# Kernel optimization log

Hardware: AMD Instinct MI355X
Metric: run time of the kernel (lower is better)

## Reference

```python
import jax, jax.numpy as jnp
import numpy as np

F_BINS, T_STEPS, N_ACTIONS = 257, 65536, 256  # STFT bins, frames, codebook size


def setup_inputs() -> dict:
    key = jax.random.key(0)
    k1, k2, k3, k4 = jax.random.split(key, 4)
    x_out = jax.random.normal(k1, (F_BINS, T_STEPS), dtype=jnp.float32)
    x_source = jax.random.normal(k2, (F_BINS, T_STEPS), dtype=jnp.float32)
    x_clean = jax.random.normal(k3, (F_BINS, T_STEPS), dtype=jnp.float32)
    # G is self.G_mat = G_mat.T, i.e. [freq, action]; gains in [0,1)
    G = jax.random.uniform(k4, (F_BINS, N_ACTIONS), dtype=jnp.float32)
    return {"x_out": x_out, "x_source": x_source, "x_clean": x_clean, "G": G}


def reference(x_out, x_source, x_clean, G):
    # sums[t, a] = sum_f (x_clean[f, t] - G[f, a] * x_source[f, t])
    #            = sum_f x_clean[:, t]  -  (x_source^T @ G)[t, a]
    clean_sum = jnp.sum(x_clean, axis=0)                 # [T]
    proj = jnp.einsum('ft,fa->ta', x_source, G)          # [T, A]
    sums = clean_sum[:, None] - proj                     # [T, A]
    A_t = jnp.argmin(sums, axis=1)                       # [T], values in [0, A)
    F, T = x_source.shape
    # Faithful to the original loop: wiener_true[:, a] = G[:, a] for each
    # SELECTED ACTION a (column indexed by action id, not timestep).
    # Duplicate indices write identical values, so scatter-set is well-defined.
    wiener_true = jnp.zeros((F, T), dtype=x_source.dtype).at[:, A_t].set(G[:, A_t])
    true_out = (wiener_true * x_source).T                # [T, F]
    loss = jnp.mean((true_out - x_out.T) ** 2)
    return loss
```

## Files before the change

kernel.cpp:

```cpp
#include <hip/hip_runtime.h>

#define F_BINS  257
#define T_STEPS 65536
#define N_ACT   256
#define TM      128
#define NBLK_G  512
#define NTHR    256
#define XO_PB   8224

typedef float f32x4 __attribute__((ext_vector_type(4)));
typedef short s16x8 __attribute__((ext_vector_type(8)));
typedef unsigned u32x4 __attribute__((ext_vector_type(4)));

#define WS_PART  1024
#define WS_CORR  20480
#define WS_MASK  24576
#define WS_GFRAG 65536

__device__ __forceinline__ unsigned short f2bf_rne(float x) {
  unsigned u = __builtin_bit_cast(unsigned, x);
  return (unsigned short)((u + 0x7FFFu + ((u >> 16) & 1u)) >> 16);
}
__device__ __forceinline__ unsigned pack_bf(float hi, float lo) {
  return __builtin_amdgcn_perm(__builtin_bit_cast(unsigned, hi),
                               __builtin_bit_cast(unsigned, lo), 0x07060302u);
}

__global__ __launch_bounds__(256) void k_prep(const float* __restrict__ G,
                                              unsigned char* __restrict__ gfrag) {
  const int u = blockIdx.x * 256 + threadIdx.x;
  const int lane = u & 63, ng = (u >> 6) & 15, kk = u >> 10;
  const int r16 = lane & 15, g = lane >> 4;
  const int a = ng * 16 + r16;
  unsigned short h[8];
#pragma unroll
  for (int j = 0; j < 8; ++j) {
    const int f = kk * 32 + 8 * g + j;
    h[j] = (f < F_BINS) ? f2bf_rne(G[f * N_ACT + a]) : (unsigned short)0;
  }
  u32x4 w;
#pragma unroll
  for (int i = 0; i < 4; ++i)
    w[i] = (unsigned)h[2 * i] | ((unsigned)h[2 * i + 1] << 16);
  *(u32x4*)(gfrag + (size_t)u * 16) = w;
}

__global__ __launch_bounds__(NTHR, 2) void k_gemm(
    const float* __restrict__ xs, const float4* __restrict__ xo4,
    const unsigned char* __restrict__ gfrag,
    unsigned* __restrict__ maskp, double* __restrict__ partial) {
  const int tid = threadIdx.x, lane = tid & 63, wv = tid >> 6;
  const int g = lane >> 4, r16 = lane & 15;
  const int t0 = blockIdx.x * TM;
  const int tcol = t0 + 32 * wv + 2 * r16;

  __shared__ __align__(16) unsigned char Bh[73728];
  __shared__ unsigned lmask[8];
  __shared__ double sdw[4];
  if (tid < 8) lmask[tid] = 0u;

#define STAGE_BH(hv)                                                          \
  {                                                                           \
    _Pragma("unroll") for (int idx = 0; idx < 18; ++idx) {                    \
      const int j = 18 * wv + idx;                      \
      const int kkc = j >> 3, ic = j & 7;                                     \
      const unsigned char* src = gfrag +                                      \
          (size_t)(kkc * 16 + 8 * (hv) + ic) * 1024 + (size_t)lane * 16;      \
      unsigned char* dst = &Bh[j * 1024];                                     \
      __builtin_amdgcn_global_load_lds(                                       \
          (const __attribute__((address_space(1))) unsigned*)src,             \
          (__attribute__((address_space(3))) unsigned*)dst, 16, 0, 0);        \
    }                                                                         \
  }
#define LOADB(slot, kkv)                                                      \
  {                                                                           \
    _Pragma("unroll") for (int j = 0; j < 8; ++j) {                           \
      int f = 32 * (kkv) + 8 * g + j;                                         \
      if ((kkv) == 8) f = f > 256 ? 256 : f;   \
      va[slot][j] = *(const float2*)(xs + (size_t)f * T_STEPS + tcol);        \
    }                                                                         \
  }

  float2 va[4][8];
  LOADB(0, 0) LOADB(1, 1) LOADB(2, 2) LOADB(3, 3)
  __builtin_amdgcn_sched_barrier(0);
  STAGE_BH(0)
  __builtin_amdgcn_sched_barrier(0);

  s16x8 af[9][2];
#pragma unroll
  for (int kk = 0; kk < 9; ++kk) {
    const int b = kk & 3;
    af[kk][0] = __builtin_bit_cast(s16x8, (u32x4){
        pack_bf(va[b][1].x, va[b][0].x), pack_bf(va[b][3].x, va[b][2].x),
        pack_bf(va[b][5].x, va[b][4].x), pack_bf(va[b][7].x, va[b][6].x)});
    af[kk][1] = __builtin_bit_cast(s16x8, (u32x4){
        pack_bf(va[b][1].y, va[b][0].y), pack_bf(va[b][3].y, va[b][2].y),
        pack_bf(va[b][5].y, va[b][4].y), pack_bf(va[b][7].y, va[b][6].y)});
    if (kk + 4 <= 8) LOADB(b, kk + 4)
  }
#undef LOADB

  __syncthreads();

  float bv[2][4]; int bc[2][4];
#pragma unroll
  for (int h = 0; h < 2; ++h) {
    if (h == 1) {
      __syncthreads();
      STAGE_BH(1)
      __syncthreads();
    }
    f32x4 acc[2][8];
#pragma unroll
    for (int tau = 0; tau < 2; ++tau)
#pragma unroll
      for (int n = 0; n < 8; ++n) acc[tau][n] = (f32x4){0.f, 0.f, 0.f, 0.f};
#pragma unroll
    for (int kk = 0; kk < 9; ++kk) {
      const unsigned char* bp = &Bh[(kk * 8 * 64 + lane) * 16];
#pragma unroll
      for (int n = 0; n < 8; ++n) {
        const s16x8 bfr = *(const s16x8*)(bp + n * 1024);
        acc[0][n] = __builtin_amdgcn_mfma_f32_16x16x32_bf16(
            af[kk][0], bfr, acc[0][n], 0, 0, 0);
        acc[1][n] = __builtin_amdgcn_mfma_f32_16x16x32_bf16(
            af[kk][1], bfr, acc[1][n], 0, 0, 0);
      }
    }
#pragma unroll
    for (int n = 0; n < 8; ++n) {
      const int c = 128 * h + 16 * n + r16;
#pragma unroll
      for (int tau = 0; tau < 2; ++tau)
#pragma unroll
        for (int q = 0; q < 4; ++q) {
          const float v = acc[tau][n][q];
          if (h == 0 && n == 0) { bv[tau][q] = v; bc[tau][q] = c; }
          else if (v > bv[tau][q]) { bv[tau][q] = v; bc[tau][q] = c; }
        }
    }
  }
#undef STAGE_BH

  const float4* xop = xo4 + (size_t)blockIdx.x * XO_PB + tid;
  float4 xv[2][8];
#pragma unroll
  for (int j = 0; j < 8; ++j) xv[0][j] = xop[j * 256];
#pragma unroll
  for (int j = 0; j < 8; ++j) xv[1][j] = xop[2048 + j * 256];
  float4 wrem = (float4){0.f, 0.f, 0.f, 0.f};
  if (tid < 32) wrem = xo4[(size_t)blockIdx.x * XO_PB + 8192 + tid];

#pragma unroll
  for (int m = 1; m <= 8; m <<= 1) {
#pragma unroll
    for (int tau = 0; tau < 2; ++tau)
#pragma unroll
      for (int q = 0; q < 4; ++q) {
        const float ov = __shfl_xor(bv[tau][q], m);
        const int   oc = __shfl_xor(bc[tau][q], m);
        if (ov > bv[tau][q] || (ov == bv[tau][q] && oc < bc[tau][q])) {
          bv[tau][q] = ov; bc[tau][q] = oc;
        }
      }
  }
  if (r16 == 0) {
#pragma unroll
    for (int tau = 0; tau < 2; ++tau)
#pragma unroll
      for (int q = 0; q < 4; ++q)
        atomicOr(&lmask[bc[tau][q] >> 5], 1u << (bc[tau][q] & 31));
  }
  __syncthreads();
  if (tid < 8) maskp[blockIdx.x * 8 + tid] = lmask[tid];

  double ds = 0.0;
#pragma unroll
  for (int r = 0; r < 4; ++r) {
    float fs = 0.f;
#pragma unroll
    for (int j = 0; j < 8; ++j) {
      const float4 v = xv[r & 1][j];
      fs = fmaf(v.x, v.x, fs); fs = fmaf(v.y, v.y, fs);
      fs = fmaf(v.z, v.z, fs); fs = fmaf(v.w, v.w, fs);
    }
    ds += (double)fs;
    if (r + 2 < 4) {
#pragma unroll
      for (int j = 0; j < 8; ++j)
        xv[r & 1][j] = xop[(size_t)(r + 2) * 2048 + j * 256];
    }
  }
  {
    float fs = 0.f;
    fs = fmaf(wrem.x, wrem.x, fs); fs = fmaf(wrem.y, wrem.y, fs);
    fs = fmaf(wrem.z, wrem.z, fs); fs = fmaf(wrem.w, wrem.w, fs);
    ds += (double)fs;
  }
#pragma unroll
  for (int off = 32; off; off >>= 1) ds += __shfl_down(ds, off);
  if (lane == 0) sdw[wv] = ds;
  __syncthreads();
  if (tid == 0) partial[blockIdx.x] = sdw[0] + sdw[1] + sdw[2] + sdw[3];
}

__global__ __launch_bounds__(256) void k_corr(
    const float* __restrict__ xs, const float* __restrict__ xo,
    const float* __restrict__ G, const unsigned* __restrict__ maskp,
    double* __restrict__ corrp) {
  __shared__ unsigned m8[8];
  const int tid = threadIdx.x;
  if (tid < 8) m8[tid] = 0u;
  __syncthreads();
  unsigned m = 0;
  for (int b = tid >> 3; b < NBLK_G; b += 32) m |= maskp[b * 8 + (tid & 7)];
  atomicOr(&m8[tid & 7], m);
  __syncthreads();
  const int f = blockIdx.x, a = tid;
  const bool sel = (m8[a >> 5] >> (a & 31)) & 1u;
  const float gv  = G[f * N_ACT + a];
  const float xsv = xs[(size_t)f * T_STEPS + a];
  const float xov = xo[(size_t)f * T_STEPS + a];
  const float gx  = gv * xsv;
  double acc = sel ? (double)(gx * (gx - 2.f * xov)) : 0.0;
#pragma unroll
  for (int off = 32; off; off >>= 1) acc += __shfl_down(acc, off);
  __shared__ double sdc[4];
  if ((tid & 63) == 0) sdc[tid >> 6] = acc;
  __syncthreads();
  if (tid == 0) corrp[f] = sdc[0] + sdc[1] + sdc[2] + sdc[3];
}

__global__ __launch_bounds__(256) void k_final(const double* __restrict__ partial,
                                               const double* __restrict__ corrp,
                                               float* __restrict__ out) {
  const int tid = threadIdx.x;
  double s = partial[tid] + partial[tid + 256] + corrp[tid];
  if (tid == 0) s += corrp[256];
#pragma unroll
  for (int off = 32; off; off >>= 1) s += __shfl_down(s, off);
  __shared__ double sd[4];
  if ((tid & 63) == 0) sd[tid >> 6] = s;
  __syncthreads();
  if (tid == 0)
    out[0] = (float)((sd[0] + sd[1] + sd[2] + sd[3]) /
                     ((double)F_BINS * (double)T_STEPS));
}

extern "C" void kernel_launch(void* const* d_in, const int* in_sizes, int n_in,
                              void* d_out, int out_size, void* d_ws, size_t ws_size,
                              hipStream_t stream) {
  const float* x_out    = (const float*)d_in[0];
  const float* x_source = (const float*)d_in[1];
  const float* G        = (const float*)d_in[3];

  char* ws = (char*)d_ws;
  double*        partial = (double*)(ws + WS_PART);
  double*        corrp   = (double*)(ws + WS_CORR);
  unsigned*      maskp   = (unsigned*)(ws + WS_MASK);
  unsigned char* gfrag   = (unsigned char*)(ws + WS_GFRAG);

  k_prep <<<36, 256, 0, stream>>>(G, gfrag);
  k_gemm <<<NBLK_G, NTHR, 0, stream>>>(x_source, (const float4*)x_out,
                                       gfrag, maskp, partial);
  k_corr <<<F_BINS, 256, 0, stream>>>(x_source, x_out, G, maskp, corrp);
  k_final<<<1, 256, 0, stream>>>(partial, corrp, (float*)d_out);
}
```

Before: 40.63 us.

## Precompute per-action correction terms in prep kernel and drop separate corr kernel

The per-action correction term no longer depends on the selection mask, so it is now computed ahead of the GEMM in extra blocks of the prep kernel, as partial sums over groups of 17 frequency bins. The mask is applied only in the final single-block reduction, which sums the 16 partial rows per action. This removes one kernel launch (the 257-block corr kernel) and its serial dependency after the GEMM. In exchange the final kernel does a bit more work and the prep kernel reads more data.

```diff
diff --git a/kernel.cpp b/kernel.cpp
--- a/kernel.cpp
+++ b/kernel.cpp
@@ -7,14 +7,16 @@
 #define NBLK_G  512
 #define NTHR    256
 #define XO_PB   8224
+#define PREP_BLKS 36
+#define CORR_BLKS 16
 
 typedef float f32x4 __attribute__((ext_vector_type(4)));
 typedef short s16x8 __attribute__((ext_vector_type(8)));
 typedef unsigned u32x4 __attribute__((ext_vector_type(4)));
 
 #define WS_PART  1024
-#define WS_CORR  20480
-#define WS_MASK  24576
+#define WS_CPART 8192
+#define WS_MASK  40960
 #define WS_GFRAG 65536
 
 __device__ __forceinline__ unsigned short f2bf_rne(float x) {
@@ -26,23 +28,42 @@
                                __builtin_bit_cast(unsigned, lo), 0x07060302u);
 }
 
-__global__ __launch_bounds__(256) void k_prep(const float* __restrict__ G,
-                                              unsigned char* __restrict__ gfrag) {
-  const int u = blockIdx.x * 256 + threadIdx.x;
-  const int lane = u & 63, ng = (u >> 6) & 15, kk = u >> 10;
-  const int r16 = lane & 15, g = lane >> 4;
-  const int a = ng * 16 + r16;
-  unsigned short h[8];
-#pragma unroll
-  for (int j = 0; j < 8; ++j) {
-    const int f = kk * 32 + 8 * g + j;
-    h[j] = (f < F_BINS) ? f2bf_rne(G[f * N_ACT + a]) : (unsigned short)0;
-  }
-  u32x4 w;
-#pragma unroll
-  for (int i = 0; i < 4; ++i)
-    w[i] = (unsigned)h[2 * i] | ((unsigned)h[2 * i + 1] << 16);
-  *(u32x4*)(gfrag + (size_t)u * 16) = w;
+__global__ __launch_bounds__(256) void k_pre(
+    const float* __restrict__ G, const float* __restrict__ xs,
+    const float* __restrict__ xo, unsigned char* __restrict__ gfrag,
+    double* __restrict__ cpart) {
+  const int tid = threadIdx.x;
+  if (blockIdx.x < PREP_BLKS) {
+    const int u = blockIdx.x * 256 + tid;
+    const int lane = u & 63, ng = (u >> 6) & 15, kk = u >> 10;
+    const int r16 = lane & 15, g = lane >> 4;
+    const int a = ng * 16 + r16;
+    unsigned short h[8];
+#pragma unroll
+    for (int j = 0; j < 8; ++j) {
+      const int f = kk * 32 + 8 * g + j;
+      h[j] = (f < F_BINS) ? f2bf_rne(G[f * N_ACT + a]) : (unsigned short)0;
+    }
+    u32x4 w;
+#pragma unroll
+    for (int i = 0; i < 4; ++i)
+      w[i] = (unsigned)h[2 * i] | ((unsigned)h[2 * i + 1] << 16);
+    *(u32x4*)(gfrag + (size_t)u * 16) = w;
+    return;
+  }
+  const int b = blockIdx.x - PREP_BLKS;
+  const int a = tid;
+  const int f0 = b * 17;
+  const int f1 = f0 + 17 > F_BINS ? F_BINS : f0 + 17;
+  double ca = 0.0;
+  for (int f = f0; f < f1; ++f) {
+    const float gv  = G[f * N_ACT + a];
+    const float xsv = xs[(size_t)f * T_STEPS + a];
+    const float xov = xo[(size_t)f * T_STEPS + a];
+    const float gx  = gv * xsv;
+    ca += (double)(gx * (gx - 2.f * xov));
+  }
+  cpart[b * 256 + a] = ca;
 }
 
 __global__ __launch_bounds__(NTHR, 2) void k_gemm(
@@ -205,10 +226,9 @@
   if (tid == 0) partial[blockIdx.x] = sdw[0] + sdw[1] + sdw[2] + sdw[3];
 }
 
-__global__ __launch_bounds__(256) void k_corr(
-    const float* __restrict__ xs, const float* __restrict__ xo,
-    const float* __restrict__ G, const unsigned* __restrict__ maskp,
-    double* __restrict__ corrp) {
+__global__ __launch_bounds__(256) void k_final(
+    const double* __restrict__ partial, const double* __restrict__ cpart,
+    const unsigned* __restrict__ maskp, float* __restrict__ out) {
   __shared__ unsigned m8[8];
   const int tid = threadIdx.x;
   if (tid < 8) m8[tid] = 0u;
@@ -217,27 +237,12 @@
   for (int b = tid >> 3; b < NBLK_G; b += 32) m |= maskp[b * 8 + (tid & 7)];
   atomicOr(&m8[tid & 7], m);
   __syncthreads();
-  const int f = blockIdx.x, a = tid;
+  const int a = tid;
   const bool sel = (m8[a >> 5] >> (a & 31)) & 1u;
-  const float gv  = G[f * N_ACT + a];
-  const float xsv = xs[(size_t)f * T_STEPS + a];
-  const float xov = xo[(size_t)f * T_STEPS + a];
-  const float gx  = gv * xsv;
-  double acc = sel ? (double)(gx * (gx - 2.f * xov)) : 0.0;
-#pragma unroll
-  for (int off = 32; off; off >>= 1) acc += __shfl_down(acc, off);
-  __shared__ double sdc[4];
-  if ((tid & 63) == 0) sdc[tid >> 6] = acc;
-  __syncthreads();
-  if (tid == 0) corrp[f] = sdc[0] + sdc[1] + sdc[2] + sdc[3];
-}
-
-__global__ __launch_bounds__(256) void k_final(const double* __restrict__ partial,
-                                               const double* __restrict__ corrp,
-                                               float* __restrict__ out) {
-  const int tid = threadIdx.x;
-  double s = partial[tid] + partial[tid + 256] + corrp[tid];
-  if (tid == 0) s += corrp[256];
+  double c = 0.0;
+#pragma unroll
+  for (int i = 0; i < CORR_BLKS; ++i) c += cpart[i * 256 + a];
+  double s = partial[tid] + partial[tid + 256] + (sel ? c : 0.0);
 #pragma unroll
   for (int off = 32; off; off >>= 1) s += __shfl_down(s, off);
   __shared__ double sd[4];
@@ -257,13 +262,13 @@
 
   char* ws = (char*)d_ws;
   double*        partial = (double*)(ws + WS_PART);
-  double*        corrp   = (double*)(ws + WS_CORR);
+  double*        cpart   = (double*)(ws + WS_CPART);
   unsigned*      maskp   = (unsigned*)(ws + WS_MASK);
   unsigned char* gfrag   = (unsigned char*)(ws + WS_GFRAG);
 
-  k_prep <<<36, 256, 0, stream>>>(G, gfrag);
+  k_pre  <<<PREP_BLKS + CORR_BLKS, 256, 0, stream>>>(G, x_source, x_out,
+                                                     gfrag, cpart);
   k_gemm <<<NBLK_G, NTHR, 0, stream>>>(x_source, (const float4*)x_out,
                                        gfrag, maskp, partial);
-  k_corr <<<F_BINS, 256, 0, stream>>>(x_source, x_out, G, maskp, corrp);
-  k_final<<<1, 256, 0, stream>>>(partial, corrp, (float*)d_out);
-}
+  k_final<<<1, 256, 0, stream>>>(partial, cpart, maskp, (float*)d_out);
+}
```

Result: no change. 40.48 us (-0.4%).
